# Optimization experiments

Hardware: AMD Instinct MI355X
Metric: run time of the kernel (lower is better)

## Reference

```python
import jax, jax.numpy as jnp
import numpy as np

N_NODES = 50000
N_EDGES = 600000
N_RELS = 16
N_GRAPHS = 128
IN_DIM = 128
REL_LAYERS = [128, 256, 128]
HIDDEN = [128, 256, 128]
N_CLASSES = 8


def setup_inputs() -> dict:
    key = jax.random.key(0)
    ks = jax.random.split(key, 24)
    inp = {}
    inp["h"] = jax.random.normal(ks[0], (N_NODES, IN_DIM), dtype=jnp.float32)
    inp["src"] = jax.random.randint(ks[1], (N_EDGES,), 0, N_NODES)
    inp["dst"] = jax.random.randint(ks[2], (N_EDGES,), 0, N_NODES)
    inp["rel_types"] = jax.random.randint(ks[3], (N_EDGES,), 0, N_RELS)
    inp["graph_ids"] = jnp.sort(jax.random.randint(ks[4], (N_NODES,), 0, N_GRAPHS))
    # RelGraphConv params per layer: W_rel [R,din,dout], W_loop [din,dout], b [dout]
    prev = IN_DIM
    ki = 5
    for i, d in enumerate(REL_LAYERS):
        inp[f"W_rel{i}"] = jax.random.normal(ks[ki], (N_RELS, prev, d), dtype=jnp.float32) * 0.05
        inp[f"W_loop{i}"] = jax.random.normal(ks[ki + 1], (prev, d), dtype=jnp.float32) * 0.05
        inp[f"b{i}"] = jnp.zeros((d,), dtype=jnp.float32)
        prev = d
        ki += 2
    for i, d in enumerate(HIDDEN):
        inp[f"Wh{i}"] = jax.random.normal(ks[ki], (prev, d), dtype=jnp.float32) * 0.05
        inp[f"bh{i}"] = jnp.zeros((d,), dtype=jnp.float32)
        prev = d
        ki += 1
    inp["Wc"] = jax.random.normal(ks[ki], (prev, N_CLASSES), dtype=jnp.float32) * 0.05
    inp["bc"] = jnp.zeros((N_CLASSES,), dtype=jnp.float32)
    return inp


def _rel_graph_conv(h, src, dst, rel, W_rel, W_loop, b):
    # transform every node under every relation: [R, N, dout]
    t = jnp.einsum("nd,rde->rne", h, W_rel)
    msgs = t[rel, src]  # [E, dout] gather per edge
    agg = jax.ops.segment_sum(msgs, dst, num_segments=h.shape[0])
    return jax.nn.relu(agg + h @ W_loop + b)  # self-loop + bias (DGL defaults)


def _forward(h, src, dst, rel_types, graph_ids,
             W_rel0, W_loop0, b0, W_rel1, W_loop1, b1, W_rel2, W_loop2, b2,
             Wh0, bh0, Wh1, bh1, Wh2, bh2, Wc, bc):
    h = h.astype(jnp.float32)
    for Wr, Wl, b in ((W_rel0, W_loop0, b0), (W_rel1, W_loop1, b1), (W_rel2, W_loop2, b2)):
        h = _rel_graph_conv(h, src, dst, rel_types, Wr, Wl, b)
    # dgl.mean_nodes: per-graph mean pooling
    sums = jax.ops.segment_sum(h, graph_ids, num_segments=N_GRAPHS)
    cnts = jax.ops.segment_sum(jnp.ones((h.shape[0],), h.dtype), graph_ids, num_segments=N_GRAPHS)
    hg = sums / jnp.maximum(cnts, 1.0)[:, None]
    for W, b in ((Wh0, bh0), (Wh1, bh1), (Wh2, bh2)):
        hg = jax.nn.relu(hg @ W + b)
    return jax.nn.softmax(hg @ Wc + bc, axis=1)


def reference(h, src, dst, rel_types, graph_ids,
              W_rel0, W_loop0, b0, W_rel1, W_loop1, b1, W_rel2, W_loop2, b2,
              Wh0, bh0, Wh1, bh1, Wh2, bh2, Wc, bc):
    return _forward(h, src, dst, rel_types, graph_ids,
                    W_rel0, W_loop0, b0, W_rel1, W_loop1, b1, W_rel2, W_loop2, b2,
                    Wh0, bh0, Wh1, bh1, Wh2, bh2, Wc, bc)
```

## Files before the change

kernel.cpp:

```cpp
#include <hip/hip_runtime.h>
#include <stdint.h>

#define NN 50000
#define NE 600000
#define NR 16
#define NG 128
#define TS 128
#define MAXB 1024

typedef short bf16x8 __attribute__((ext_vector_type(8)));
typedef float f32x4 __attribute__((ext_vector_type(4)));

static __device__ __forceinline__ unsigned short f2bf(float x) {
    unsigned int b = __float_as_uint(x);
    b += 0x7FFFu + ((b >> 16) & 1u);
    return (unsigned short)(b >> 16);
}
static __device__ __forceinline__ float bf2f(unsigned short u) {
    return __uint_as_float(((unsigned int)u) << 16);
}


__global__ void k_zero(int* bcnt, int* cursor, int* ncnt, int* ncur, float* hg, float* gcnt) {
    int i = blockIdx.x * 256 + threadIdx.x;
    if (i < MAXB) { bcnt[i] = 0; cursor[i] = 0; }
    if (i < NN) { ncnt[i] = 0; ncur[i] = 0; }
    if (i < NG * 128) hg[i] = 0.f;
    if (i < NG) gcnt[i] = 0.f;
}

__global__ void k_hist(const int* __restrict__ rel, const int* __restrict__ dst,
                       int* __restrict__ bcnt, int* __restrict__ ncnt, int npc, int B) {
    __shared__ int lh[MAXB];
    for (int i = threadIdx.x; i < B; i += 256) lh[i] = 0;
    __syncthreads();
    for (int e = blockIdx.x * blockDim.x + threadIdx.x; e < NE; e += gridDim.x * blockDim.x) {
        int d = dst[e];
        atomicAdd(&lh[(d / npc) * NR + rel[e]], 1);
        atomicAdd(&ncnt[d], 1);
    }
    __syncthreads();
    for (int i = threadIdx.x; i < B; i += 256) atomicAdd(&bcnt[i], lh[i]);
}

__global__ __launch_bounds__(1024)
void k_nodescan(const int* __restrict__ ncnt, int* __restrict__ rowptr) {
    __shared__ int s[1024];
    const int per = (NN + 1023) / 1024;
    int tid = threadIdx.x;
    int base = tid * per;
    int lim = base + per; if (lim > NN) lim = NN;
    int sum = 0;
    for (int i = base; i < lim; ++i) sum += ncnt[i];
    s[tid] = sum;
    __syncthreads();
    for (int off = 1; off < 1024; off <<= 1) {
        int x = (tid >= off) ? s[tid - off] : 0;
        __syncthreads();
        s[tid] += x;
        __syncthreads();
    }
    int run = s[tid] - sum;
    for (int i = base; i < lim; ++i) { rowptr[i] = run; run += ncnt[i]; }
    if (tid == 1023) rowptr[NN] = s[1023];
}

__global__ __launch_bounds__(1024)
void k_scan_buckets(const int* __restrict__ bcnt, int B, int npc,
                    const int* __restrict__ rowptr,
                    int* __restrict__ boff, int* __restrict__ tstart,
                    int4* __restrict__ tilemap) {
    __shared__ int s1[MAXB], s2[MAXB];
    int tid = threadIdx.x;
    int v1 = (tid < B) ? bcnt[tid] : 0;
    int v2 = (v1 + TS - 1) / TS;
    s1[tid] = v1; s2[tid] = v2;
    __syncthreads();
    for (int off = 1; off < MAXB; off <<= 1) {
        int a1 = (tid >= off) ? s1[tid - off] : 0;
        int a2 = (tid >= off) ? s2[tid - off] : 0;
        __syncthreads();
        s1[tid] += a1; s2[tid] += a2;
        __syncthreads();
    }
    if (tid < B) {
        int e0b = s1[tid] - v1;
        int t0  = s2[tid] - v2;
        boff[tid] = e0b;
        tstart[tid] = t0;
        if (tid == B - 1) { boff[B] = s1[tid]; tstart[B] = s2[tid]; }
        int relr = tid & (NR - 1);
        int chunk = tid >> 4;
        int nstart = chunk * npc; if (nstart > NN) nstart = NN;
        int cES = rowptr[nstart];
        for (int tt = 0; tt < v2; ++tt) {
            int rem = v1 - tt * TS;
            int cnt = rem < TS ? rem : TS;
            tilemap[t0 + tt] = make_int4(relr, e0b + tt * TS, cnt, cES);
        }
    }
}

__global__ void k_scatter(const int* __restrict__ rel, const int* __restrict__ dst,
                          const int* __restrict__ boff, int* __restrict__ cursor,
                          const int* __restrict__ rowptr, int* __restrict__ ncur,
                          int* __restrict__ sorted, int* __restrict__ dpos, int npc, int B) {
    __shared__ int lh[MAXB];
    const int CH = 4096;
    int e0 = blockIdx.x * CH;
    for (int i = threadIdx.x; i < B; i += 256) lh[i] = 0;
    __syncthreads();
    for (int i = threadIdx.x; i < CH; i += 256) {
        int e = e0 + i;
        if (e < NE) atomicAdd(&lh[(dst[e] / npc) * NR + rel[e]], 1);
    }
    __syncthreads();
    for (int i = threadIdx.x; i < B; i += 256) {
        int c = lh[i];
        lh[i] = (c > 0) ? atomicAdd(&cursor[i], c) : 0;
    }
    __syncthreads();
    for (int i = threadIdx.x; i < CH; i += 256) {
        int e = e0 + i;
        if (e < NE) {
            int d = dst[e];
            int b = (d / npc) * NR + rel[e];
            int p = boff[b] + atomicAdd(&lh[b], 1);
            int pd = rowptr[d] + atomicAdd(&ncur[d], 1);
            sorted[p] = e;
            dpos[p] = pd;
        }
    }
}


__global__ void k_hconv(const float* __restrict__ h, unsigned short* __restrict__ hb, int n4) {
    int i = blockIdx.x * 256 + threadIdx.x;
    if (i < n4) {
        float4 v = reinterpret_cast<const float4*>(h)[i];
        ushort4 o = { f2bf(v.x), f2bf(v.y), f2bf(v.z), f2bf(v.w) };
        reinterpret_cast<ushort4*>(hb)[i] = o;
    }
}

__global__ void k_wconv_all(const float* Wr0, const float* Wr1, const float* Wr2,
                            const float* Wl0, const float* Wl1, const float* Wl2,
                            unsigned short* Wt0, unsigned short* Wt1, unsigned short* Wt2,
                            unsigned short* Wlt0, unsigned short* Wlt1, unsigned short* Wlt2) {
    const float* W; unsigned short* O; int R, Kd, Nd;
    switch (blockIdx.y) {
        case 0:  W = Wr0; O = Wt0;  R = NR; Kd = 128; Nd = 128; break;
        case 1:  W = Wr1; O = Wt1;  R = NR; Kd = 128; Nd = 256; break;
        case 2:  W = Wr2; O = Wt2;  R = NR; Kd = 256; Nd = 128; break;
        case 3:  W = Wl0; O = Wlt0; R = 1;  Kd = 128; Nd = 128; break;
        case 4:  W = Wl1; O = Wlt1; R = 1;  Kd = 128; Nd = 256; break;
        default: W = Wl2; O = Wlt2; R = 1;  Kd = 256; Nd = 128; break;
    }
    int total = R * Kd * Nd;
    for (int i = blockIdx.x * 256 + threadIdx.x; i < total; i += gridDim.x * 256) {
        int r = i / (Kd * Nd);
        int rem = i - r * Kd * Nd;
        int k = rem / Nd;
        int n = rem - k * Nd;
        O[((size_t)r * Nd + n) * Kd + k] = f2bf(W[i]);
    }
}


template<int K>
__global__ __launch_bounds__(256, 4)
void k_dense_mfma(const unsigned short* __restrict__ hb,
                  const unsigned short* __restrict__ Wlt,
                  const float* __restrict__ bias,
                  float* __restrict__ outbuf, int ldn) {
    __shared__ __align__(16) unsigned short As[128][72];
    __shared__ __align__(16) unsigned short Bs[128][72];
    const int tid = threadIdx.x;
    const int row0 = blockIdx.x * 128;
    const int colbase = blockIdx.y * 128;
    const int lane = tid & 63, w = tid >> 6;
    const int quad = lane >> 4, col = lane & 15;
    const int srow = tid >> 3, sk = (tid & 7) * 8;

    f32x4 acc[8][2];
#pragma unroll
    for (int i = 0; i < 8; ++i) { acc[i][0] = 0.f; acc[i][1] = 0.f; }

    for (int k0 = 0; k0 < K; k0 += 64) {
        __syncthreads();
#pragma unroll
        for (int pp = 0; pp < 4; ++pp) {
            int rw = pp * 32 + srow;
            int ar = row0 + rw; if (ar >= NN) ar = NN - 1;
            *reinterpret_cast<uint4*>(&As[rw][sk]) =
                *reinterpret_cast<const uint4*>(hb + (size_t)ar * K + k0 + sk);
            *reinterpret_cast<uint4*>(&Bs[rw][sk]) =
                *reinterpret_cast<const uint4*>(Wlt + (size_t)(colbase + rw) * K + k0 + sk);
        }
        __syncthreads();
#pragma unroll
        for (int s = 0; s < 2; ++s) {
            bf16x8 bf0 = *reinterpret_cast<const bf16x8*>(&Bs[w * 32 + col][s * 32 + quad * 8]);
            bf16x8 bf1 = *reinterpret_cast<const bf16x8*>(&Bs[w * 32 + 16 + col][s * 32 + quad * 8]);
#pragma unroll
            for (int rt = 0; rt < 8; ++rt) {
                bf16x8 af = *reinterpret_cast<const bf16x8*>(&As[rt * 16 + col][s * 32 + quad * 8]);
                acc[rt][0] = __builtin_amdgcn_mfma_f32_16x16x32_bf16(af, bf0, acc[rt][0], 0, 0, 0);
                acc[rt][1] = __builtin_amdgcn_mfma_f32_16x16x32_bf16(af, bf1, acc[rt][1], 0, 0, 0);
            }
        }
    }
    float bv0 = bias[colbase + w * 32 + col];
    float bv1 = bias[colbase + w * 32 + 16 + col];
#pragma unroll
    for (int rt = 0; rt < 8; ++rt) {
#pragma unroll
        for (int reg = 0; reg < 4; ++reg) {
            int r = row0 + rt * 16 + quad * 4 + reg;
            if (r < NN) {
                float* dp = outbuf + (size_t)r * ldn + colbase + w * 32;
                dp[col] = acc[rt][0][reg] + bv0;
                dp[16 + col] = acc[rt][1][reg] + bv1;
            }
        }
    }
}


template<int K>
__global__ __launch_bounds__(256, 4)
void k_edge_mfma(const unsigned short* __restrict__ hb,
                 const unsigned short* __restrict__ Wt,
                 int ldn, int colbase,
                 const int* __restrict__ src,
                 const int* __restrict__ sorted, const int* __restrict__ dpos,
                 const int4* __restrict__ tilemap, const int* __restrict__ tstart,
                 int chunkBase,
                 unsigned short* __restrict__ msg, int capRows) {
    const int tb0 = tstart[chunkBase];
    const int tend = tstart[chunkBase + NR];
    const int t = tb0 + blockIdx.x;
    if (t >= tend) return;
    const int4 tm = tilemap[t];
    const int r = tm.x, e0 = tm.y, cnt = tm.z, cES = tm.w;

    __shared__ __align__(16) unsigned short As[128][136];
    __shared__ int s_src[TS], s_out[TS];
    const int tid = threadIdx.x;
    if (tid < TS) {
        int ei = e0 + (tid < cnt ? tid : cnt - 1);
        int e = sorted[ei];
        s_src[tid] = src[e];
        int row = dpos[ei] - cES;
        s_out[tid] = (tid < cnt && row < capRows) ? row : -1;
    }
    __syncthreads();

    const unsigned short* Wb = Wt + ((size_t)r * ldn + colbase) * K;
    const int lane = tid & 63, w = tid >> 6;
    const int quad = lane >> 4, col = lane & 15;
    const int asr = tid >> 4, ask = (tid & 15) * 8;

    f32x4 acc[8][2];
#pragma unroll
    for (int i = 0; i < 8; ++i) { acc[i][0] = 0.f; acc[i][1] = 0.f; }

    for (int kk = 0; kk < K; kk += 128) {
        if (kk) __syncthreads();
#pragma unroll
        for (int q = 0; q < 8; ++q) {
            int rw = q * 16 + asr;
            *reinterpret_cast<uint4*>(&As[rw][ask]) =
                *reinterpret_cast<const uint4*>(hb + (size_t)s_src[rw] * K + kk + ask);
        }
        __syncthreads();
#pragma unroll
        for (int k32 = 0; k32 < 4; ++k32) {
            bf16x8 bf0 = *reinterpret_cast<const bf16x8*>(
                Wb + (size_t)(w * 32 + col) * K + kk + k32 * 32 + quad * 8);
            bf16x8 bf1 = *reinterpret_cast<const bf16x8*>(
                Wb + (size_t)(w * 32 + 16 + col) * K + kk + k32 * 32 + quad * 8);
#pragma unroll
            for (int rt = 0; rt < 8; ++rt) {
                bf16x8 af = *reinterpret_cast<const bf16x8*>(&As[rt * 16 + col][k32 * 32 + quad * 8]);
                acc[rt][0] = __builtin_amdgcn_mfma_f32_16x16x32_bf16(af, bf0, acc[rt][0], 0, 0, 0);
                acc[rt][1] = __builtin_amdgcn_mfma_f32_16x16x32_bf16(af, bf1, acc[rt][1], 0, 0, 0);
            }
        }
    }
#pragma unroll
    for (int rt = 0; rt < 8; ++rt) {
#pragma unroll
        for (int reg = 0; reg < 4; ++reg) {
            int m = rt * 16 + quad * 4 + reg;
            int o = s_out[m];
            if (o >= 0) {
                unsigned short* dp = msg + (size_t)o * 128 + w * 32;
                dp[col] = f2bf(acc[rt][0][reg]);
                dp[16 + col] = f2bf(acc[rt][1][reg]);
            }
        }
    }
}

__global__ __launch_bounds__(256)
void k_reduce(const unsigned short* __restrict__ msg,
              const float* __restrict__ selfb, int ld_self, int co_self,
              unsigned short* __restrict__ out_bf, int ld_bf, int co_bf,
              float* __restrict__ out_f32, int ld_f32, int co_f32,
              const int* __restrict__ rowptr, int n0, int npc, int capRows) {
    int idx = blockIdx.x * 4 + (threadIdx.x >> 6);
    int n = n0 + idx;
    if (idx >= npc || n >= NN) return;
    int lane = threadIdx.x & 63;
    int cES = rowptr[n0];
    float2 acc = *reinterpret_cast<const float2*>(selfb + (size_t)n * ld_self + co_self + lane * 2);
    int j0 = rowptr[n], j1 = rowptr[n + 1];
    for (int j = j0; j < j1; ++j) {
        int rr = j - cES;
        if (rr >= capRows) break;
        unsigned int m = *reinterpret_cast<const unsigned int*>(msg + (size_t)rr * 128 + lane * 2);
        acc.x += bf2f((unsigned short)(m & 0xffffu));
        acc.y += bf2f((unsigned short)(m >> 16));
    }
    acc.x = acc.x > 0.f ? acc.x : 0.f;
    acc.y = acc.y > 0.f ? acc.y : 0.f;
    if (out_bf) {
        unsigned int o = (unsigned int)f2bf(acc.x) | ((unsigned int)f2bf(acc.y) << 16);
        *reinterpret_cast<unsigned int*>(out_bf + (size_t)n * ld_bf + co_bf + lane * 2) = o;
    }
    if (out_f32) {
        *reinterpret_cast<float2*>(out_f32 + (size_t)n * ld_f32 + co_f32 + lane * 2) = acc;
    }
}


__global__ void k_pool(const float* __restrict__ h, const int* __restrict__ gid,
                       float* __restrict__ hg, float* __restrict__ gcnt) {
    const int c = threadIdx.x;
    int n0 = blockIdx.x * 64;
    if (n0 >= NN) return;
    int end = n0 + 64; if (end > NN) end = NN;
    int cur = gid[n0];
    float run = 0.f, crun = 0.f;
    for (int n = n0; n < end; ++n) {
        int g = gid[n];
        if (g != cur) {
            atomicAdd(&hg[cur * 128 + c], run);
            if (c == 0) atomicAdd(&gcnt[cur], crun);
            run = 0.f; crun = 0.f; cur = g;
        }
        run += h[(size_t)n * 128 + c];
        crun += 1.f;
    }
    atomicAdd(&hg[cur * 128 + c], run);
    if (c == 0) atomicAdd(&gcnt[cur], crun);
}

__global__ __launch_bounds__(256)
void k_head(const float* __restrict__ hg, const float* __restrict__ gcnt,
            const float* __restrict__ Wh0, const float* __restrict__ bh0,
            const float* __restrict__ Wh1, const float* __restrict__ bh1,
            const float* __restrict__ Wh2, const float* __restrict__ bh2,
            const float* __restrict__ Wc, const float* __restrict__ bc,
            float* __restrict__ out) {
    __shared__ float x0[128], x1[128], x2[256], x3[128], sl[8];
    int g = blockIdx.x, t = threadIdx.x;
    if (t < 128) {
        float c = gcnt[g];
        x0[t] = hg[g * 128 + t] / (c > 1.f ? c : 1.f);
    }
    __syncthreads();
    if (t < 128) {
        float a = bh0[t];
        for (int k = 0; k < 128; ++k) a += x0[k] * Wh0[k * 128 + t];
        x1[t] = a > 0.f ? a : 0.f;
    }
    __syncthreads();
    {
        float a = bh1[t];
        for (int k = 0; k < 128; ++k) a += x1[k] * Wh1[k * 256 + t];
        x2[t] = a > 0.f ? a : 0.f;
    }
    __syncthreads();
    if (t < 128) {
        float a = bh2[t];
        for (int k = 0; k < 256; ++k) a += x2[k] * Wh2[k * 128 + t];
        x3[t] = a > 0.f ? a : 0.f;
    }
    __syncthreads();
    if (t < 8) {
        float a = bc[t];
        for (int k = 0; k < 128; ++k) a += x3[k] * Wc[k * 8 + t];
        sl[t] = a;
    }
    __syncthreads();
    if (t == 0) {
        float m = sl[0];
        for (int c = 1; c < 8; ++c) m = sl[c] > m ? sl[c] : m;
        float s = 0.f, e[8];
        for (int c = 0; c < 8; ++c) { e[c] = expf(sl[c] - m); s += e[c]; }
        for (int c = 0; c < 8; ++c) out[g * 8 + c] = e[c] / s;
    }
}


extern "C" void kernel_launch(void* const* d_in, const int* in_sizes, int n_in,
                              void* d_out, int out_size, void* d_ws, size_t ws_size,
                              hipStream_t stream) {
    const float* h0   = (const float*)d_in[0];
    const int* src    = (const int*)d_in[1];
    const int* dst    = (const int*)d_in[2];
    const int* rel    = (const int*)d_in[3];
    const int* gid    = (const int*)d_in[4];
    const float* Wr0  = (const float*)d_in[5];
    const float* Wl0  = (const float*)d_in[6];
    const float* b0   = (const float*)d_in[7];
    const float* Wr1  = (const float*)d_in[8];
    const float* Wl1  = (const float*)d_in[9];
    const float* b1   = (const float*)d_in[10];
    const float* Wr2  = (const float*)d_in[11];
    const float* Wl2  = (const float*)d_in[12];
    const float* b2   = (const float*)d_in[13];
    const float* Wh0  = (const float*)d_in[14];
    const float* bh0  = (const float*)d_in[15];
    const float* Wh1  = (const float*)d_in[16];
    const float* bh1  = (const float*)d_in[17];
    const float* Wh2  = (const float*)d_in[18];
    const float* bh2  = (const float*)d_in[19];
    const float* Wc   = (const float*)d_in[20];
    const float* bc   = (const float*)d_in[21];
    float* out = (float*)d_out;

    char* p = (char*)d_ws;
    auto alloc = [&](size_t bytes) { char* q = p; p += (bytes + 255) & ~(size_t)255; return q; };
    float* bufS  = (float*)alloc((size_t)NN * 256 * 4);
    unsigned short* hbA = (unsigned short*)alloc((size_t)NN * 256 * 2);
    unsigned short* hbB = (unsigned short*)alloc((size_t)NN * 128 * 2);
    unsigned short* Wt0 = (unsigned short*)alloc((size_t)NR * 128 * 128 * 2);
    unsigned short* Wt1 = (unsigned short*)alloc((size_t)NR * 256 * 128 * 2);
    unsigned short* Wt2 = (unsigned short*)alloc((size_t)NR * 128 * 256 * 2);
    unsigned short* Wlt0 = (unsigned short*)alloc((size_t)128 * 128 * 2);
    unsigned short* Wlt1 = (unsigned short*)alloc((size_t)256 * 128 * 2);
    unsigned short* Wlt2 = (unsigned short*)alloc((size_t)128 * 256 * 2);
    int* sorted  = (int*)alloc((size_t)NE * 4);
    int* dpos    = (int*)alloc((size_t)NE * 4);
    int* ncnt    = (int*)alloc((size_t)NN * 4);
    int* ncur    = (int*)alloc((size_t)NN * 4);
    int* rowptr  = (int*)alloc((size_t)(NN + 1) * 4);
    int* bcnt    = (int*)alloc(MAXB * 4);
    int* boff    = (int*)alloc((MAXB + 1) * 4);
    int* tstart  = (int*)alloc((MAXB + 1) * 4);
    int* cursor  = (int*)alloc(MAXB * 4);
    int4* tilemap = (int4*)alloc((size_t)(NE / TS + MAXB + 64) * 16);
    float* hg    = (float*)alloc((size_t)NG * 128 * 4);
    float* gcnt  = (float*)alloc(NG * 4);
    unsigned short* msg = (unsigned short*)p;

    long long avail = (long long)ws_size - (long long)(p - (char*)d_ws);
    if (avail < (1 << 20)) avail = (1 << 20);
    long long capR64 = avail / 256;
    int C = 64;
    for (int c = 1; c <= 64; ++c) {
        double need = (double)NE / c * 1.15 + 4096.0;
        if ((double)capR64 >= need) { C = c; break; }
    }
    int npc = (NN + C - 1) / C;
    int B = C * NR;
    int capRows = capR64 > 2000000000LL ? 2000000000 : (int)capR64;
    int TPC = (int)((double)NE / C * 1.15 / TS) + NR + 8;
    int RDB = (npc + 3) / 4;

    k_zero<<<(NN + 255) / 256, 256, 0, stream>>>(bcnt, cursor, ncnt, ncur, hg, gcnt);
    k_hist<<<256, 256, 0, stream>>>(rel, dst, bcnt, ncnt, npc, B);
    k_nodescan<<<1, 1024, 0, stream>>>(ncnt, rowptr);
    k_scan_buckets<<<1, MAXB, 0, stream>>>(bcnt, B, npc, rowptr, boff, tstart, tilemap);
    k_scatter<<<(NE + 4095) / 4096, 256, 0, stream>>>(rel, dst, boff, cursor, rowptr, ncur, sorted, dpos, npc, B);

    k_hconv<<<(NN * 128 / 4 + 255) / 256, 256, 0, stream>>>(h0, hbA, NN * 128 / 4);
    k_wconv_all<<<dim3(512, 6), 256, 0, stream>>>(Wr0, Wr1, Wr2, Wl0, Wl1, Wl2,
                                                  Wt0, Wt1, Wt2, Wlt0, Wlt1, Wlt2);

    const int RB = (NN + TS - 1) / TS;

    k_dense_mfma<128><<<dim3(RB, 1), 256, 0, stream>>>(hbA, Wlt0, b0, bufS, 128);
    for (int c = 0; c < C; ++c) {
        k_edge_mfma<128><<<TPC, 256, 0, stream>>>(hbA, Wt0, 128, 0, src, sorted, dpos, tilemap, tstart, c * NR, msg, capRows);
        k_reduce<<<RDB, 256, 0, stream>>>(msg, bufS, 128, 0, hbB, 128, 0, (float*)nullptr, 0, 0, rowptr, c * npc, npc, capRows);
    }

    k_dense_mfma<128><<<dim3(RB, 2), 256, 0, stream>>>(hbB, Wlt1, b1, bufS, 256);
    for (int half = 0; half < 2; ++half) {
        for (int c = 0; c < C; ++c) {
            k_edge_mfma<128><<<TPC, 256, 0, stream>>>(hbB, Wt1, 256, half * 128, src, sorted, dpos, tilemap, tstart, c * NR, msg, capRows);
            k_reduce<<<RDB, 256, 0, stream>>>(msg, bufS, 256, half * 128, hbA, 256, half * 128, (float*)nullptr, 0, 0, rowptr, c * npc, npc, capRows);
        }
    }

    k_dense_mfma<256><<<dim3(RB, 1), 256, 0, stream>>>(hbA, Wlt2, b2, bufS, 128);
    for (int c = 0; c < C; ++c) {
        k_edge_mfma<256><<<TPC, 256, 0, stream>>>(hbA, Wt2, 128, 0, src, sorted, dpos, tilemap, tstart, c * NR, msg, capRows);
        k_reduce<<<RDB, 256, 0, stream>>>(msg, bufS, 128, 0, (unsigned short*)nullptr, 0, 0, bufS, 128, 0, rowptr, c * npc, npc, capRows);
    }

    k_pool<<<(NN + 63) / 64, 128, 0, stream>>>(bufS, gid, hg, gcnt);
    k_head<<<NG, 256, 0, stream>>>(hg, gcnt, Wh0, bh0, Wh1, bh1, Wh2, bh2, Wc, bc, out);
}
```

Before: 919.6 us.

## Parallelize node scan, tilemap fill, and pre-resolve sorted src indices

Replaces the single-block node prefix scan with a three-kernel multi-block scan. The bucket tilemap is now filled by all threads, each binary-searching its bucket, instead of a per-bucket serial loop. The scatter stores src[e] directly, so edge kernels drop one dependent indirect load per edge. This targets the serial preprocessing and gather latency, at the cost of two extra kernel launches and a serial single-thread pass over about 98 block sums.

```diff
diff --git a/kernel.cpp b/kernel.cpp
--- a/kernel.cpp
+++ b/kernel.cpp
@@ -6,6 +6,8 @@
 #define NR 16
 #define NG 128
 #define TS 128
+#define SCAN_B 512
+#define NB_SCAN ((NN + SCAN_B - 1) / SCAN_B)
 #define MAXB 1024
 
 typedef short bf16x8 __attribute__((ext_vector_type(8)));
@@ -43,26 +45,40 @@
     for (int i = threadIdx.x; i < B; i += 256) atomicAdd(&bcnt[i], lh[i]);
 }
 
-__global__ __launch_bounds__(1024)
-void k_nodescan(const int* __restrict__ ncnt, int* __restrict__ rowptr) {
-    __shared__ int s[1024];
-    const int per = (NN + 1023) / 1024;
-    int tid = threadIdx.x;
-    int base = tid * per;
-    int lim = base + per; if (lim > NN) lim = NN;
-    int sum = 0;
-    for (int i = base; i < lim; ++i) sum += ncnt[i];
-    s[tid] = sum;
-    __syncthreads();
-    for (int off = 1; off < 1024; off <<= 1) {
-        int x = (tid >= off) ? s[tid - off] : 0;
-        __syncthreads();
-        s[tid] += x;
-        __syncthreads();
-    }
-    int run = s[tid] - sum;
-    for (int i = base; i < lim; ++i) { rowptr[i] = run; run += ncnt[i]; }
-    if (tid == 1023) rowptr[NN] = s[1023];
+__global__ void k_scan1(const int* __restrict__ ncnt, int* __restrict__ bsum) {
+    __shared__ int s[SCAN_B];
+    int i = blockIdx.x * SCAN_B + threadIdx.x;
+    s[threadIdx.x] = (i < NN) ? ncnt[i] : 0;
+    __syncthreads();
+    for (int off = SCAN_B / 2; off > 0; off >>= 1) {
+        if (threadIdx.x < off) s[threadIdx.x] += s[threadIdx.x + off];
+        __syncthreads();
+    }
+    if (threadIdx.x == 0) bsum[blockIdx.x] = s[0];
+}
+
+__global__ void k_scan2(const int* __restrict__ bsum, int* __restrict__ bpref, int* __restrict__ rowptr) {
+    if (threadIdx.x == 0 && blockIdx.x == 0) {
+        int run = 0;
+        for (int b = 0; b < NB_SCAN; ++b) { bpref[b] = run; run += bsum[b]; }
+        rowptr[NN] = run;
+    }
+}
+
+__global__ void k_scan3(const int* __restrict__ ncnt, const int* __restrict__ bpref,
+                        int* __restrict__ rowptr) {
+    __shared__ int s[SCAN_B];
+    int i = blockIdx.x * SCAN_B + threadIdx.x;
+    int val = (i < NN) ? ncnt[i] : 0;
+    s[threadIdx.x] = val;
+    __syncthreads();
+    for (int off = 1; off < SCAN_B; off <<= 1) {
+        int x = (threadIdx.x >= off) ? s[threadIdx.x - off] : 0;
+        __syncthreads();
+        s[threadIdx.x] += x;
+        __syncthreads();
+    }
+    if (i < NN) rowptr[i] = bpref[blockIdx.x] + s[threadIdx.x] - val;
 }
 
 __global__ __launch_bounds__(1024)
@@ -71,6 +87,7 @@
                     int* __restrict__ boff, int* __restrict__ tstart,
                     int4* __restrict__ tilemap) {
     __shared__ int s1[MAXB], s2[MAXB];
+    __shared__ int e_ex[MAXB + 1], t_ex[MAXB + 1];
     int tid = threadIdx.x;
     int v1 = (tid < B) ? bcnt[tid] : 0;
     int v2 = (v1 + TS - 1) / TS;
@@ -84,27 +101,39 @@
         __syncthreads();
     }
     if (tid < B) {
-        int e0b = s1[tid] - v1;
-        int t0  = s2[tid] - v2;
-        boff[tid] = e0b;
-        tstart[tid] = t0;
-        if (tid == B - 1) { boff[B] = s1[tid]; tstart[B] = s2[tid]; }
-        int relr = tid & (NR - 1);
-        int chunk = tid >> 4;
+        e_ex[tid] = s1[tid] - v1;
+        t_ex[tid] = s2[tid] - v2;
+        boff[tid] = e_ex[tid];
+        tstart[tid] = t_ex[tid];
+        if (tid == B - 1) {
+            e_ex[B] = s1[tid]; t_ex[B] = s2[tid];
+            boff[B] = s1[tid]; tstart[B] = s2[tid];
+        }
+    }
+    __syncthreads();
+    int T = t_ex[B];
+    for (int t = tid; t < T; t += 1024) {
+        int lo = 0, hi = B - 1;
+        while (lo < hi) {
+            int mid = (lo + hi + 1) >> 1;
+            if (t_ex[mid] <= t) lo = mid; else hi = mid - 1;
+        }
+        int b = lo;
+        int tt = t - t_ex[b];
+        int v1b = e_ex[b + 1] - e_ex[b];
+        int rem = v1b - tt * TS;
+        int cnt = rem < TS ? rem : TS;
+        int chunk = b >> 4;
         int nstart = chunk * npc; if (nstart > NN) nstart = NN;
-        int cES = rowptr[nstart];
-        for (int tt = 0; tt < v2; ++tt) {
-            int rem = v1 - tt * TS;
-            int cnt = rem < TS ? rem : TS;
-            tilemap[t0 + tt] = make_int4(relr, e0b + tt * TS, cnt, cES);
-        }
+        tilemap[t] = make_int4(b & (NR - 1), e_ex[b] + tt * TS, cnt, rowptr[nstart]);
     }
 }
 
 __global__ void k_scatter(const int* __restrict__ rel, const int* __restrict__ dst,
+                          const int* __restrict__ src,
                           const int* __restrict__ boff, int* __restrict__ cursor,
                           const int* __restrict__ rowptr, int* __restrict__ ncur,
-                          int* __restrict__ sorted, int* __restrict__ dpos, int npc, int B) {
+                          int* __restrict__ srcs, int* __restrict__ dpos, int npc, int B) {
     __shared__ int lh[MAXB];
     const int CH = 4096;
     int e0 = blockIdx.x * CH;
@@ -127,7 +156,7 @@
             int b = (d / npc) * NR + rel[e];
             int p = boff[b] + atomicAdd(&lh[b], 1);
             int pd = rowptr[d] + atomicAdd(&ncur[d], 1);
-            sorted[p] = e;
+            srcs[p] = src[e];
             dpos[p] = pd;
         }
     }
@@ -232,8 +261,7 @@
 void k_edge_mfma(const unsigned short* __restrict__ hb,
                  const unsigned short* __restrict__ Wt,
                  int ldn, int colbase,
-                 const int* __restrict__ src,
-                 const int* __restrict__ sorted, const int* __restrict__ dpos,
+                 const int* __restrict__ srcs, const int* __restrict__ dpos,
                  const int4* __restrict__ tilemap, const int* __restrict__ tstart,
                  int chunkBase,
                  unsigned short* __restrict__ msg, int capRows) {
@@ -249,8 +277,7 @@
     const int tid = threadIdx.x;
     if (tid < TS) {
         int ei = e0 + (tid < cnt ? tid : cnt - 1);
-        int e = sorted[ei];
-        s_src[tid] = src[e];
+        s_src[tid] = srcs[ei];
         int row = dpos[ei] - cES;
         s_out[tid] = (tid < cnt && row < capRows) ? row : -1;
     }
@@ -443,11 +470,13 @@
     unsigned short* Wlt0 = (unsigned short*)alloc((size_t)128 * 128 * 2);
     unsigned short* Wlt1 = (unsigned short*)alloc((size_t)256 * 128 * 2);
     unsigned short* Wlt2 = (unsigned short*)alloc((size_t)128 * 256 * 2);
-    int* sorted  = (int*)alloc((size_t)NE * 4);
+    int* srcs    = (int*)alloc((size_t)NE * 4);
     int* dpos    = (int*)alloc((size_t)NE * 4);
     int* ncnt    = (int*)alloc((size_t)NN * 4);
     int* ncur    = (int*)alloc((size_t)NN * 4);
     int* rowptr  = (int*)alloc((size_t)(NN + 1) * 4);
+    int* bsum    = (int*)alloc(NB_SCAN * 4);
+    int* bpref   = (int*)alloc(NB_SCAN * 4);
     int* bcnt    = (int*)alloc(MAXB * 4);
     int* boff    = (int*)alloc((MAXB + 1) * 4);
     int* tstart  = (int*)alloc((MAXB + 1) * 4);
@@ -473,9 +502,11 @@
 
     k_zero<<<(NN + 255) / 256, 256, 0, stream>>>(bcnt, cursor, ncnt, ncur, hg, gcnt);
     k_hist<<<256, 256, 0, stream>>>(rel, dst, bcnt, ncnt, npc, B);
-    k_nodescan<<<1, 1024, 0, stream>>>(ncnt, rowptr);
+    k_scan1<<<NB_SCAN, SCAN_B, 0, stream>>>(ncnt, bsum);
+    k_scan2<<<1, 64, 0, stream>>>(bsum, bpref, rowptr);
+    k_scan3<<<NB_SCAN, SCAN_B, 0, stream>>>(ncnt, bpref, rowptr);
     k_scan_buckets<<<1, MAXB, 0, stream>>>(bcnt, B, npc, rowptr, boff, tstart, tilemap);
-    k_scatter<<<(NE + 4095) / 4096, 256, 0, stream>>>(rel, dst, boff, cursor, rowptr, ncur, sorted, dpos, npc, B);
+    k_scatter<<<(NE + 4095) / 4096, 256, 0, stream>>>(rel, dst, src, boff, cursor, rowptr, ncur, srcs, dpos, npc, B);
 
     k_hconv<<<(NN * 128 / 4 + 255) / 256, 256, 0, stream>>>(h0, hbA, NN * 128 / 4);
     k_wconv_all<<<dim3(512, 6), 256, 0, stream>>>(Wr0, Wr1, Wr2, Wl0, Wl1, Wl2,
@@ -485,21 +516,21 @@
 
     k_dense_mfma<128><<<dim3(RB, 1), 256, 0, stream>>>(hbA, Wlt0, b0, bufS, 128);
     for (int c = 0; c < C; ++c) {
-        k_edge_mfma<128><<<TPC, 256, 0, stream>>>(hbA, Wt0, 128, 0, src, sorted, dpos, tilemap, tstart, c * NR, msg, capRows);
+        k_edge_mfma<128><<<TPC, 256, 0, stream>>>(hbA, Wt0, 128, 0, srcs, dpos, tilemap, tstart, c * NR, msg, capRows);
         k_reduce<<<RDB, 256, 0, stream>>>(msg, bufS, 128, 0, hbB, 128, 0, (float*)nullptr, 0, 0, rowptr, c * npc, npc, capRows);
     }
 
     k_dense_mfma<128><<<dim3(RB, 2), 256, 0, stream>>>(hbB, Wlt1, b1, bufS, 256);
     for (int half = 0; half < 2; ++half) {
         for (int c = 0; c < C; ++c) {
-            k_edge_mfma<128><<<TPC, 256, 0, stream>>>(hbB, Wt1, 256, half * 128, src, sorted, dpos, tilemap, tstart, c * NR, msg, capRows);
+            k_edge_mfma<128><<<TPC, 256, 0, stream>>>(hbB, Wt1, 256, half * 128, srcs, dpos, tilemap, tstart, c * NR, msg, capRows);
             k_reduce<<<RDB, 256, 0, stream>>>(msg, bufS, 256, half * 128, hbA, 256, half * 128, (float*)nullptr, 0, 0, rowptr, c * npc, npc, capRows);
         }
     }
 
     k_dense_mfma<256><<<dim3(RB, 1), 256, 0, stream>>>(hbA, Wlt2, b2, bufS, 128);
     for (int c = 0; c < C; ++c) {
-        k_edge_mfma<256><<<TPC, 256, 0, stream>>>(hbA, Wt2, 128, 0, src, sorted, dpos, tilemap, tstart, c * NR, msg, capRows);
+        k_edge_mfma<256><<<TPC, 256, 0, stream>>>(hbA, Wt2, 128, 0, srcs, dpos, tilemap, tstart, c * NR, msg, capRows);
         k_reduce<<<RDB, 256, 0, stream>>>(msg, bufS, 128, 0, (unsigned short*)nullptr, 0, 0, bufS, 128, 0, rowptr, c * npc, npc, capRows);
     }
 
```

New measurement: 829.4 us. 1.11x faster.
